# Performance work log

Hardware: AMD Instinct MI355X
Metric: run time of the kernel (lower is better)

Reference implementation:

```python
import jax, jax.numpy as jnp
import numpy as np

CONF_THRES = 0.5   # self.conf_thres
NMS_THRES = 0.5    # self.nms_thres
PRE_NMS = 2048     # candidates kept before pairwise IoU
MAX_DET = 300      # padded detections returned per image
MAX_WH = 4096.0    # class-offset trick so NMS is per-class
IMG_SIZE = 416.0   # self.img_size; boxes_scale (416,416)->(416,416) => scale 1


def xywh2xyxy(b):
    xy, wh = b[..., :2], b[..., 2:4]
    return jnp.concatenate([xy - wh * 0.5, xy + wh * 0.5], axis=-1)


def pairwise_iou(boxes):
    # boxes: [K,4] xyxy -> [K,K] IoU
    area = (boxes[:, 2] - boxes[:, 0]) * (boxes[:, 3] - boxes[:, 1])
    lt = jnp.maximum(boxes[:, None, :2], boxes[None, :, :2])
    rb = jnp.minimum(boxes[:, None, 2:], boxes[None, :, 2:])
    wh = jnp.clip(rb - lt, 0.0)
    inter = wh[..., 0] * wh[..., 1]
    return inter / (area[:, None] + area[None, :] - inter + 1e-16)


def nms_single(pred):
    # pred: [N,85] = xywh(4) + objectness(1) + class scores(80)
    boxes = xywh2xyxy(pred[:, :4])
    obj = pred[:, 4]
    cls_scores = pred[:, 5:] * obj[:, None]        # conf = obj * class prob
    conf = jnp.max(cls_scores, axis=-1)
    cls_id = jnp.argmax(cls_scores, axis=-1)
    valid = obj >= CONF_THRES                      # confidence threshold filter
    score = jnp.where(valid, conf, -1.0)

    order = jnp.argsort(-score)[:PRE_NMS]          # sort desc, keep top PRE_NMS
    boxes_s = boxes[order]
    score_s = score[order]
    cls_s = cls_id[order]
    valid_s = valid[order]

    # per-class NMS via coordinate offset by class id
    off = cls_s.astype(boxes_s.dtype) * MAX_WH
    iou = pairwise_iou(boxes_s + off[:, None])     # [PRE_NMS, PRE_NMS]

    def body(keep, i):
        suppressed = jnp.any(keep & (iou[:, i] > NMS_THRES))
        k = valid_s[i] & ~suppressed
        return keep.at[i].set(k), k

    keep, _ = jax.lax.scan(body, jnp.zeros(PRE_NMS, dtype=bool), jnp.arange(PRE_NMS))

    final_score = jnp.where(keep, score_s, -1.0)
    top = jnp.argsort(-final_score)[:MAX_DET]
    kb, ks, kc, km = boxes_s[top], score_s[top], cls_s[top], keep[top]

    scale = IMG_SIZE / 416.0                       # boxes_scale (identity here)
    det = jnp.concatenate(
        [kb * scale, ks[:, None], kc[:, None].astype(kb.dtype)], axis=-1)
    return jnp.where(km[:, None], det, 0.0)        # [MAX_DET, 6] padded


def setup_inputs() -> dict:
    key = jax.random.key(0)
    predictions = jax.random.uniform(key, (16, 10647, 85), dtype=jnp.float32)
    return {"predictions": predictions}


def reference(predictions):
    # detections per image: [x1,y1,x2,y2,score,class], zero-padded to MAX_DET
    return jax.vmap(nms_single)(predictions)  # [B, MAX_DET, 6]
```

## Files before the change

kernel.cpp:

```cpp
#include <hip/hip_runtime.h>
#include <hip/hip_bf16.h>
#include <stdint.h>

typedef unsigned long long u64;
typedef unsigned int u32;
typedef unsigned short u16;

#define NANCH 10647
#define NBATCH 16
#define NSORT 16384
#define NSEL 2048
#define NWORD 32
#define NCLS 80
#define CONF_T 0.5f
#define NMS_T 0.5f
#define MAXDET 300
#define MAXWH 4096.0f
#define CANDCAP 10688
#define PART 1344
#define NBLK1 84

__device__ __forceinline__ float dec_score(u64 key) {
    u32 v = ~(u32)(key >> 32);
    u32 u = (v & 0x80000000u) ? (v & 0x7FFFFFFFu) : ~v;
    return __uint_as_float(u);
}

__global__ __launch_bounds__(256) void k_prep(const float* __restrict__ pred,
                                              u64* __restrict__ keys,
                                              float4* __restrict__ boxes,
                                              int* __restrict__ cls,
                                              u32* __restrict__ bhist,
                                              u32* __restrict__ ghist2) {
    __shared__ float sm[128 * 85];
    __shared__ u32 ph[256];
    int b = blockIdx.y;
    if (blockIdx.x == 0) ghist2[(size_t)b * 256 + threadIdx.x] = 0;
    int a0 = blockIdx.x * 128;
    int na = NANCH - a0; if (na > 128) na = 128;
    const float* src = pred + ((size_t)b * NANCH + a0) * 85;
    int tot = na * 85;
    ph[threadIdx.x] = 0;
    {
        size_t srcaddr = (size_t)src;
        int shift = (int)((srcaddr & 15) >> 2);
        const float4* A = (const float4*)(srcaddr & ~(size_t)15);
        int nvec = (tot + shift + 3) >> 2;
        for (int j = threadIdx.x; j < nvec; j += 256) {
            float4 v = A[j];
            int base = 4 * j - shift;
            if (base >= 0 && base + 3 < tot) {
                sm[base] = v.x; sm[base + 1] = v.y;
                sm[base + 2] = v.z; sm[base + 3] = v.w;
            } else {
                if (base >= 0 && base < tot)         sm[base]     = v.x;
                if (base + 1 >= 0 && base + 1 < tot) sm[base + 1] = v.y;
                if (base + 2 >= 0 && base + 2 < tot) sm[base + 2] = v.z;
                if (base + 3 >= 0 && base + 3 < tot) sm[base + 3] = v.w;
            }
        }
    }
    __syncthreads();
    int t = threadIdx.x;
    u64 kk = 0;
    if (t < na) {
        const float* s = &sm[t * 85];
        float x = s[0], y = s[1], w = s[2], h = s[3], obj = s[4];
        float best = s[5] * obj; int arg = 0;
        #pragma unroll
        for (int c = 1; c < 80; ++c) {
            float v = s[5 + c] * obj;
            if (v > best) { best = v; arg = c; }
        }
        bool valid = obj >= CONF_T;
        float sc = valid ? best : -1.0f;
        int a = a0 + t;
        float4 bx;
        bx.x = x - w * 0.5f; bx.y = y - h * 0.5f;
        bx.z = x + w * 0.5f; bx.w = y + h * 0.5f;
        size_t o = (size_t)b * NANCH + a;
        boxes[o] = bx;
        cls[o] = arg;
        u32 u = __float_as_uint(sc);
        u32 v = (u & 0x80000000u) ? ~u : (u | 0x80000000u);
        u32 hi = ~v;
        kk = ((u64)hi << 32) | (u32)a;
        keys[(size_t)b * NSORT + a] = kk;
    }
    u32 bin = (t < na) ? (u32)(kk >> 56) : 0xFFFFFFFFu;
    int lane = t & 63;
    u64 rem = __ballot(t < na);
    while (rem) {
        int srcl = __ffsll((long long)rem) - 1;
        u32 lb = __shfl(bin, srcl);
        u64 same = __ballot(bin == lb) & rem;
        if (lane == srcl) atomicAdd(&ph[lb], (u32)__popcll(same));
        rem &= ~same;
    }
    __syncthreads();
    bhist[(((size_t)b * NBLK1) + blockIdx.x) * 256 + threadIdx.x] = ph[threadIdx.x];
}

__global__ __launch_bounds__(1024) void k_scan(const u64* __restrict__ keys,
                                               const u32* __restrict__ bhist,
                                               u64* __restrict__ gslice,
                                               uint2* __restrict__ gpart,
                                               u32* __restrict__ ghist2) {
    __shared__ u32 hist[256];
    __shared__ u32 hsc[256];
    __shared__ u32 ph2[256];
    __shared__ u32 s_D0;
    __shared__ u32 wcs[16], wcc[16];
    __shared__ u32 s_tc;
    int b = blockIdx.y;
    int part = blockIdx.x;
    int tid = threadIdx.x;
    int lane = tid & 63, wv = tid >> 6;
    u64 below = (1ULL << lane) - 1ULL;
    const u64* KB = keys + (size_t)b * NSORT;

    if (tid < 256) {
        ph2[tid] = 0;
        u32 h = 0;
        const u32* BH = bhist + (size_t)b * NBLK1 * 256 + tid;
        for (int j = 0; j < NBLK1; ++j) h += BH[(size_t)j * 256];
        hist[tid] = h;
    }
    __syncthreads();
    if (tid < 64) {
        u32 h0 = hist[tid*4], h1 = hist[tid*4+1], h2 = hist[tid*4+2], h3 = hist[tid*4+3];
        u32 loc = h0 + h1 + h2 + h3;
        u32 p = loc;
        #pragma unroll
        for (int o = 1; o < 64; o <<= 1) { u32 t2 = __shfl_up(p, o); if (lane >= o) p += t2; }
        u32 base = p - loc;
        hsc[tid*4]   = base + h0;
        hsc[tid*4+1] = base + h0 + h1;
        hsc[tid*4+2] = base + h0 + h1 + h2;
        hsc[tid*4+3] = base + h0 + h1 + h2 + h3;
    }
    __syncthreads();
    if (tid < 256) {
        u32 inc = hsc[tid], cb = inc - hist[tid];
        if (cb < NSEL && NSEL <= inc) s_D0 = tid;
    }
    __syncthreads();
    u32 D0 = s_D0;

    u64 kk0 = 0, kk1 = 0;
    bool s0 = false, s1 = false, c0 = false, c1 = false;
    {
        int off = tid, i = part * PART + off;
        bool inb = (off < PART) && (i < NANCH);
        kk0 = inb ? KB[i] : 0ULL;
        u32 top = (u32)(kk0 >> 56);
        s0 = inb && (top < D0); c0 = inb && (top == D0);
    }
    {
        int off = 1024 + tid, i = part * PART + off;
        bool inb = (off < PART) && (i < NANCH);
        kk1 = inb ? KB[i] : 0ULL;
        u32 top = (u32)(kk1 >> 56);
        s1 = inb && (top < D0); c1 = inb && (top == D0);
    }
    if (c0) atomicAdd(&ph2[(u32)(kk0 >> 48) & 0xFFu], 1u);
    if (c1) atomicAdd(&ph2[(u32)(kk1 >> 48) & 0xFFu], 1u);
    u64 bs0 = __ballot(s0), bs1 = __ballot(s1);
    u64 bc0 = __ballot(c0), bc1 = __ballot(c1);
    if (lane == 0) {
        wcs[wv] = (u32)(__popcll(bs0) + __popcll(bs1));
        wcc[wv] = (u32)(__popcll(bc0) + __popcll(bc1));
    }
    __syncthreads();
    if (tid < 16) {
        u32 vs = wcs[tid], vc = wcc[tid];
        u32 ps = vs, pc = vc;
        #pragma unroll
        for (int o = 1; o < 16; o <<= 1) {
            u32 ts = __shfl_up(ps, o);
            u32 tc = __shfl_up(pc, o);
            if (tid >= o) { ps += ts; pc += tc; }
        }
        wcs[tid] = ps - vs;
        wcc[tid] = pc - vc;
        if (tid == 15) {
            s_tc = pc;
            gpart[(size_t)b * 8 + part] = make_uint2(ps, pc);
        }
    }
    __syncthreads();
    u64* SL = gslice + ((size_t)b * 8 + part) * (size_t)PART;
    u32 base_s = wcs[wv];
    u32 base_c = (u32)PART - s_tc + wcc[wv];
    if (s0) SL[base_s + __popcll(bs0 & below)] = kk0;
    if (s1) SL[base_s + __popcll(bs0) + __popcll(bs1 & below)] = kk1;
    if (c0) SL[base_c + __popcll(bc0 & below)] = kk0;
    if (c1) SL[base_c + __popcll(bc0) + __popcll(bc1 & below)] = kk1;
    if (tid < 256 && ph2[tid]) atomicAdd(&ghist2[(size_t)b * 256 + tid], ph2[tid]);
}

__global__ __launch_bounds__(1024) void k_fin(const u64* __restrict__ gslice,
                                              const uint2* __restrict__ gpart,
                                              const u32* __restrict__ ghist2,
                                              u64* __restrict__ gskey,
                                              u64* __restrict__ gkeep) {
    __shared__ u64 sk[NSEL];
    __shared__ u64 cand[CANDCAP];
    __shared__ u32 hist[256];
    __shared__ u32 hsc[256];
    __shared__ u64 s_red[16];
    __shared__ u32 ssA[8], ccA[8];
    __shared__ u32 s_D, s_r0, s_rank, s_cnt, s_cand;

    int b = blockIdx.x;
    int tid = threadIdx.x;
    int lane = tid & 63, wv = tid >> 6;
    u64 below = (1ULL << lane) - 1ULL;

    if (tid < 8) { uint2 v = gpart[(size_t)b * 8 + tid]; ssA[tid] = v.x; ccA[tid] = v.y; }
    if (tid < 256) hist[tid] = ghist2[(size_t)b * 256 + tid];
    for (int i = tid; i < NSEL; i += 1024) sk[i] = ~0ULL;
    __syncthreads();
    if (tid == 0) {
        u32 a = 0;
        for (int j = 0; j < 8; ++j) a += ssA[j];
        s_r0 = NSEL - a;
        s_cnt = 0; s_cand = 0;
    }
    if (tid < 64) {
        u32 h0 = hist[tid*4], h1 = hist[tid*4+1], h2 = hist[tid*4+2], h3 = hist[tid*4+3];
        u32 loc = h0 + h1 + h2 + h3;
        u32 p = loc;
        #pragma unroll
        for (int o = 1; o < 64; o <<= 1) { u32 t2 = __shfl_up(p, o); if (lane >= o) p += t2; }
        u32 base = p - loc;
        hsc[tid*4]   = base + h0;
        hsc[tid*4+1] = base + h0 + h1;
        hsc[tid*4+2] = base + h0 + h1 + h2;
        hsc[tid*4+3] = base + h0 + h1 + h2 + h3;
    }
    __syncthreads();
    if (tid < 256) {
        u32 inc = hsc[tid], cb = inc - hist[tid];
        u32 r0 = s_r0;
        if (cb < r0 && r0 <= inc) s_D = tid;
    }
    __syncthreads();
    u32 D48 = s_D;

    if (wv < 8) {
        int j = wv;
        const u64* SL = gslice + ((size_t)b * 8 + j) * (size_t)PART;
        u32 ns = ssA[j];
        for (u32 i0 = 0; i0 < ns; i0 += 64) {
            u32 i = i0 + lane;
            bool act = i < ns;
            u64 kk = act ? SL[i] : 0ULL;
            u64 bal = __ballot(act);
            u32 base = 0;
            if (lane == 0) base = atomicAdd(&s_cnt, (u32)__popcll(bal));
            base = __shfl(base, 0);
            if (act) sk[base + __popcll(bal & below)] = kk;
        }
    } else {
        int j = wv - 8;
        u32 nc = ccA[j];
        const u64* SL = gslice + ((size_t)b * 8 + j) * (size_t)PART + (PART - nc);
        for (u32 i0 = 0; i0 < nc; i0 += 64) {
            u32 i = i0 + lane;
            bool act = i < nc;
            u64 kk = act ? SL[i] : 0ULL;
            u32 dg = (u32)(kk >> 48) & 0xFFu;
            bool tks = act && (dg < D48);
            bool tkc = act && (dg == D48);
            u64 bs = __ballot(tks), bc = __ballot(tkc);
            u32 base_s = 0, base_c = 0;
            if (lane == 0) {
                if (bs) base_s = atomicAdd(&s_cnt, (u32)__popcll(bs));
                if (bc) base_c = atomicAdd(&s_cand, (u32)__popcll(bc));
            }
            base_s = __shfl(base_s, 0); base_c = __shfl(base_c, 0);
            if (tks) sk[base_s + __popcll(bs & below)] = kk;
            if (tkc) cand[base_c + __popcll(bc & below)] = kk;
        }
    }
    __syncthreads();
    if (tid == 0) s_rank = NSEL - s_cnt;
    __syncthreads();

    const int shifts2[5] = {48, 40, 32, 8, 0};
    for (int rr = 1; ; ++rr) {
        u32 cn = s_cand, r = s_rank;
        if (r == cn || rr == 5) {
            for (u32 i0 = 0; i0 < cn; i0 += 1024) {
                u32 i = i0 + tid;
                bool take = i < cn;
                u64 kk = take ? cand[i] : 0ULL;
                u64 bt = __ballot(take);
                u32 base = 0;
                if (lane == 0 && bt) base = atomicAdd(&s_cnt, (u32)__popcll(bt));
                base = __shfl(base, 0);
                if (take) sk[base + __popcll(bt & below)] = kk;
            }
            break;
        }
        if (r == 1) {
            u64 best = ~0ULL;
            for (u32 i = tid; i < cn; i += 1024) { u64 kk = cand[i]; if (kk < best) best = kk; }
            #pragma unroll
            for (int o = 32; o > 0; o >>= 1) {
                u64 other = __shfl_down(best, o);
                if (other < best) best = other;
            }
            if (lane == 0) s_red[tid >> 6] = best;
            __syncthreads();
            if (tid == 0) {
                u64 m = s_red[0];
                for (int w2 = 1; w2 < 16; ++w2) if (s_red[w2] < m) m = s_red[w2];
                sk[atomicAdd(&s_cnt, 1u)] = m;
            }
            break;
        }
        int shift = shifts2[rr];
        if (tid < 256) hist[tid] = 0;
        __syncthreads();
        for (u32 i = tid; i < cn; i += 1024)
            atomicAdd(&hist[(u32)(cand[i] >> shift) & 0xFFu], 1u);
        __syncthreads();
        if (tid < 64) {
            u32 h0 = hist[tid*4], h1 = hist[tid*4+1], h2 = hist[tid*4+2], h3 = hist[tid*4+3];
            u32 loc = h0 + h1 + h2 + h3;
            u32 p = loc;
            #pragma unroll
            for (int o = 1; o < 64; o <<= 1) { u32 t2 = __shfl_up(p, o); if (lane >= o) p += t2; }
            u32 base = p - loc;
            hsc[tid*4]   = base + h0;
            hsc[tid*4+1] = base + h0 + h1;
            hsc[tid*4+2] = base + h0 + h1 + h2;
            hsc[tid*4+3] = base + h0 + h1 + h2 + h3;
        }
        __syncthreads();
        if (tid < 256) {
            u32 inc = hsc[tid], cb = inc - hist[tid];
            if (cb < r && r <= inc) { s_D = tid; s_rank = r - cb; }
        }
        __syncthreads();
        u32 D = s_D;
        u64 vv[11]; bool vb[11];
        #pragma unroll
        for (int it = 0; it < 11; ++it) {
            u32 i = tid + it * 1024;
            vb[it] = (i < cn);
            vv[it] = vb[it] ? cand[i] : 0ULL;
        }
        __syncthreads();
        if (tid == 0) s_cand = 0;
        __syncthreads();
        #pragma unroll
        for (int it = 0; it < 11; ++it) {
            u32 dg = (u32)(vv[it] >> shift) & 0xFFu;
            bool tk = vb[it] && (dg < D);
            u64 bt = __ballot(tk);
            u32 base = 0;
            if (lane == 0 && bt) base = atomicAdd(&s_cnt, (u32)__popcll(bt));
            base = __shfl(base, 0);
            if (tk) sk[base + __popcll(bt & below)] = vv[it];
        }
        #pragma unroll
        for (int it = 0; it < 11; ++it) {
            u32 dg = (u32)(vv[it] >> shift) & 0xFFu;
            bool tk = vb[it] && (dg == D);
            u64 bt = __ballot(tk);
            u32 base = 0;
            if (lane == 0 && bt) base = atomicAdd(&s_cand, (u32)__popcll(bt));
            base = __shfl(base, 0);
            if (tk) cand[base + __popcll(bt & below)] = vv[it];
        }
        __syncthreads();
    }
    __syncthreads();

    {
        int w = tid >> 6, l = lane;
        int base = w * 128;
        u64 a = sk[base + l], c = sk[base + 64 + l];
        #pragma unroll
        for (int k = 2; k <= 128; k <<= 1) {
            for (int j = k >> 1; j > 0; j >>= 1) {
                if (j == 64) {
                    bool dir = (((base + l) & k) == 0);
                    u64 lo = a < c ? a : c;
                    u64 hi = a < c ? c : a;
                    a = dir ? lo : hi;
                    c = dir ? hi : lo;
                } else {
                    bool up_ = (l & j) != 0;
                    bool dira = (((base + l) & k) == 0);
                    bool dirc = (((base + 64 + l) & k) == 0);
                    u64 pa = __shfl_xor(a, j);
                    u64 pc = __shfl_xor(c, j);
                    a = (up_ == dira) ? (a > pa ? a : pa) : (a < pa ? a : pa);
                    c = (up_ == dirc) ? (c > pc ? c : pc) : (c < pc ? c : pc);
                }
            }
        }
        sk[base + l] = a; sk[base + 64 + l] = c;
        __syncthreads();
        for (int k = 256; k <= NSEL; k <<= 1) {
            for (int j = k >> 1; j >= 128; j >>= 1) {
                int n = tid;
                int i = ((n & ~(j - 1)) << 1) | (n & (j - 1));
                int l2 = i | j;
                u64 x = sk[i], y = sk[l2];
                bool up2 = ((i & k) == 0);
                if ((x > y) == up2) { sk[i] = y; sk[l2] = x; }
                __syncthreads();
            }
            a = sk[base + l]; c = sk[base + 64 + l];
            bool dirk = ((base & k) == 0);
            {
                u64 lo = a < c ? a : c;
                u64 hi = a < c ? c : a;
                a = dirk ? lo : hi;
                c = dirk ? hi : lo;
            }
            #pragma unroll
            for (int j = 32; j > 0; j >>= 1) {
                bool up_ = (l & j) != 0;
                u64 pa = __shfl_xor(a, j);
                u64 pc = __shfl_xor(c, j);
                a = (up_ == dirk) ? (a > pa ? a : pa) : (a < pa ? a : pa);
                c = (up_ == dirk) ? (c > pc ? c : pc) : (c < pc ? c : pc);
            }
            sk[base + l] = a; sk[base + 64 + l] = c;
            __syncthreads();
        }
    }

    for (int i = tid; i < NSEL; i += 1024) gskey[(size_t)b * NSEL + i] = sk[i];
    if (tid < NWORD) gkeep[(size_t)b * NWORD + tid] = 0ULL;
}

__global__ __launch_bounds__(256) void k_gather(const u64* __restrict__ gskey,
                                                const float4* __restrict__ boxes,
                                                const int* __restrict__ cls,
                                                float4* __restrict__ sel_box,
                                                float4* __restrict__ sel_sbox,
                                                float* __restrict__ sel_area,
                                                float* __restrict__ sel_score,
                                                int* __restrict__ sel_cls) {
    int b = blockIdx.y;
    int r = blockIdx.x * 256 + threadIdx.x;
    u64 key = gskey[(size_t)b * NSEL + r];
    int a = (int)(key & 0xFFFFFFFFu);
    if ((unsigned)a >= NANCH) a = 0;
    size_t src = (size_t)b * NANCH + a;
    float4 bx = boxes[src];
    int c = cls[src];
    float sc = dec_score(key);
    float off = (float)c * MAXWH;
    float4 sb;
    sb.x = bx.x + off; sb.y = bx.y + off;
    sb.z = bx.z + off; sb.w = bx.w + off;
    float area = (sb.z - sb.x) * (sb.w - sb.y);
    size_t o = (size_t)b * NSEL + r;
    sel_box[o] = bx; sel_sbox[o] = sb; sel_area[o] = area;
    sel_score[o] = sc; sel_cls[o] = c;
}

__global__ __launch_bounds__(1024) void k_cnms(const float4* __restrict__ sel_sbox,
                                               const float* __restrict__ sel_area,
                                               const int* __restrict__ sel_cls,
                                               const float* __restrict__ sel_score,
                                               u64* __restrict__ gkeep) {
    __shared__ u16 wmem[16][NSEL];
    __shared__ u64 wkeep[16][NWORD];

    int b = blockIdx.y;
    int cg = blockIdx.x;
    int lane = threadIdx.x & 63, wv = threadIdx.x >> 6;
    int c = cg * 16 + wv;
    size_t bb = (size_t)b * NSEL;
    const int* CL = sel_cls + bb;
    const float* SC = sel_score + bb;
    u64 below = (1ULL << lane) - 1ULL;

    int n = 0;
    for (int ch = 0; ch < NWORD; ++ch) {
        int i = ch * 64 + lane;
        bool pred = (CL[i] == c) && (SC[i] >= 0.0f);
        u64 bal = __ballot(pred);
        if (pred) wmem[wv][n + __popcll(bal & below)] = (u16)i;
        n += __popcll(bal);
    }

    for (int c0 = 0; c0 < n; c0 += 64) {
        int chunkn = n - c0; if (chunkn > 64) chunkn = 64;
        bool mv = lane < chunkn;
        int q = mv ? (int)wmem[wv][c0 + lane] : 0;
        float4 bq = sel_sbox[bb + q];
        float aq = sel_area[bb + q];

        bool hit = false;
        for (int j = 0; j < c0; ++j) {
            if (!((wkeep[wv][j >> 6] >> (j & 63)) & 1ULL)) continue;
            int p = (int)wmem[wv][j];
            float4 bp = sel_sbox[bb + p];
            float ap = sel_area[bb + p];
            float ltx = fmaxf(bp.x, bq.x), lty = fmaxf(bp.y, bq.y);
            float rbx = fminf(bp.z, bq.z), rby = fminf(bp.w, bq.w);
            float ww = fmaxf(rbx - ltx, 0.0f), hh = fmaxf(rby - lty, 0.0f);
            float inter = ww * hh;
            hit = hit || (mv && (inter / (ap + aq - inter + 1e-16f) > NMS_T));
        }
        u64 avail = __ballot(mv && !hit);

        u64 Rt = 0;
        for (int t = 0; t < chunkn; ++t) {
            int p = (int)wmem[wv][c0 + t];
            float4 bp = sel_sbox[bb + p];
            float ap = sel_area[bb + p];
            float ltx = fmaxf(bp.x, bq.x), lty = fmaxf(bp.y, bq.y);
            float rbx = fminf(bp.z, bq.z), rby = fminf(bp.w, bq.w);
            float ww = fmaxf(rbx - ltx, 0.0f), hh = fmaxf(rby - lty, 0.0f);
            float inter = ww * hh;
            u64 row = __ballot(mv && (inter / (ap + aq - inter + 1e-16f) > NMS_T));
            if (lane == t) Rt = row;
        }

        u64 U = avail, kept = 0;
        while (U) {
            bool inU = ((U >> lane) & 1ULL) != 0ULL;
            u64 newk = __ballot(inU && ((Rt & U & below) == 0ULL));
            u64 killed = __ballot((Rt & newk) != 0ULL);
            kept |= newk;
            U &= ~(newk | killed);
        }
        if (lane == 0) wkeep[wv][c0 >> 6] = kept;
        if ((kept >> lane) & 1ULL)
            atomicOr(&gkeep[(size_t)b * NWORD + (q >> 6)], 1ULL << (q & 63));
    }
}

__global__ __launch_bounds__(64) void k_out(const u64* __restrict__ gkeep,
                                            const float4* __restrict__ sel_box,
                                            const float* __restrict__ sel_score,
                                            const int* __restrict__ sel_cls,
                                            float* __restrict__ out) {
    int b = blockIdx.x;
    int lane = threadIdx.x;
    const float* SC = sel_score + (size_t)b * NSEL;
    u64 kreg = (lane < NWORD) ? gkeep[(size_t)b * NWORD + lane] : 0ULL;

    int cnt = (lane < NWORD) ? __popcll(kreg) : 0;
    int pre = cnt;
    #pragma unroll
    for (int dd = 1; dd < 64; dd <<= 1) {
        int o = __shfl_up(pre, dd);
        if (lane >= dd) pre += o;
    }
    int total = __shfl(pre, 63);
    int base = pre - cnt;
    float* OUT = out + (size_t)b * MAXDET * 6;
    if (lane < NWORD) {
        u64 m = kreg;
        int rr = 0;
        while (m) {
            int t = __ffsll((long long)m) - 1;
            m &= m - 1;
            int slot = base + rr; ++rr;
            if (slot < MAXDET) {
                int i = lane * 64 + t;
                size_t src = (size_t)b * NSEL + i;
                float4 bx = sel_box[src];
                float sc = SC[i];
                int c = sel_cls[src];
                float* o6 = OUT + slot * 6;
                o6[0] = bx.x; o6[1] = bx.y; o6[2] = bx.z; o6[3] = bx.w;
                o6[4] = sc; o6[5] = (float)c;
            }
        }
    }
    int start = total > MAXDET ? MAXDET : total;
    for (int s = start + lane; s < MAXDET; s += 64) {
        float* o6 = OUT + s * 6;
        o6[0] = 0.0f; o6[1] = 0.0f; o6[2] = 0.0f;
        o6[3] = 0.0f; o6[4] = 0.0f; o6[5] = 0.0f;
    }
}

extern "C" void kernel_launch(void* const* d_in, const int* in_sizes, int n_in,
                              void* d_out, int out_size, void* d_ws, size_t ws_size,
                              hipStream_t stream) {
    const float* pred = (const float*)d_in[0];
    float* out = (float*)d_out;

    char* ws = (char*)d_ws;
    size_t off = 0;
    auto alloc = [&](size_t bytes) -> void* {
        void* p = ws + off;
        off += (bytes + 255) & ~(size_t)255;
        return p;
    };

    u64*    keys      = (u64*)   alloc((size_t)NBATCH * NSORT * 8);
    float4* boxes     = (float4*)alloc((size_t)NBATCH * NANCH * 16);
    int*    cls       = (int*)   alloc((size_t)NBATCH * NANCH * 4);
    u32*    bhist     = (u32*)   alloc((size_t)NBATCH * NBLK1 * 256 * 4);
    u32*    ghist2    = (u32*)   alloc((size_t)NBATCH * 256 * 4);
    u64*    gslice    = (u64*)   alloc((size_t)NBATCH * 8 * PART * 8);
    uint2*  gpart     = (uint2*) alloc((size_t)NBATCH * 8 * 8);
    u64*    gskey     = (u64*)   alloc((size_t)NBATCH * NSEL * 8);
    u64*    gkeep     = (u64*)   alloc((size_t)NBATCH * NWORD * 8);
    float4* sel_box   = (float4*)alloc((size_t)NBATCH * NSEL * 16);
    float4* sel_sbox  = (float4*)alloc((size_t)NBATCH * NSEL * 16);
    float*  sel_area  = (float*) alloc((size_t)NBATCH * NSEL * 4);
    float*  sel_score = (float*) alloc((size_t)NBATCH * NSEL * 4);
    int*    sel_cls   = (int*)   alloc((size_t)NBATCH * NSEL * 4);

    dim3 g1(NBLK1, NBATCH);
    k_prep<<<g1, 256, 0, stream>>>(pred, keys, boxes, cls, bhist, ghist2);

    dim3 g2(8, NBATCH);
    k_scan<<<g2, 1024, 0, stream>>>(keys, bhist, gslice, gpart, ghist2);

    k_fin<<<NBATCH, 1024, 0, stream>>>(gslice, gpart, ghist2, gskey, gkeep);

    dim3 g4(8, NBATCH);
    k_gather<<<g4, 256, 0, stream>>>(gskey, boxes, cls,
                                     sel_box, sel_sbox, sel_area,
                                     sel_score, sel_cls);

    dim3 g5(5, NBATCH);
    k_cnms<<<g5, 1024, 0, stream>>>(sel_sbox, sel_area, sel_cls, sel_score, gkeep);

    k_out<<<NBATCH, 64, 0, stream>>>(gkeep, sel_box, sel_score, sel_cls, out);
}
```

Baseline: 100.5 us.

## Fuse gather into class-NMS kernel with compacted shared-memory box staging

Removes the separate gather kernel and its intermediate selection buffers. The NMS kernel now reads sorted keys, boxes and classes directly, does a two-pass count and prefix sum to compact each class's candidates into one shared pool, and stages the offset boxes and areas in LDS. The inner IoU loops then read from shared memory instead of global memory. The output kernel decodes score, box and class from the key again. The cost is one fewer launch and less global traffic, in exchange for reading the keys twice and doing dependent global loads on the class array.

New measurement: 134.2 us. 1.33x slower.

```diff
diff --git a/kernel.cpp b/kernel.cpp
--- a/kernel.cpp
+++ b/kernel.cpp
@@ -441,72 +441,81 @@
     if (tid < NWORD) gkeep[(size_t)b * NWORD + tid] = 0ULL;
 }
 
-__global__ __launch_bounds__(256) void k_gather(const u64* __restrict__ gskey,
-                                                const float4* __restrict__ boxes,
-                                                const int* __restrict__ cls,
-                                                float4* __restrict__ sel_box,
-                                                float4* __restrict__ sel_sbox,
-                                                float* __restrict__ sel_area,
-                                                float* __restrict__ sel_score,
-                                                int* __restrict__ sel_cls) {
-    int b = blockIdx.y;
-    int r = blockIdx.x * 256 + threadIdx.x;
-    u64 key = gskey[(size_t)b * NSEL + r];
-    int a = (int)(key & 0xFFFFFFFFu);
-    if ((unsigned)a >= NANCH) a = 0;
-    size_t src = (size_t)b * NANCH + a;
-    float4 bx = boxes[src];
-    int c = cls[src];
-    float sc = dec_score(key);
-    float off = (float)c * MAXWH;
-    float4 sb;
-    sb.x = bx.x + off; sb.y = bx.y + off;
-    sb.z = bx.z + off; sb.w = bx.w + off;
-    float area = (sb.z - sb.x) * (sb.w - sb.y);
-    size_t o = (size_t)b * NSEL + r;
-    sel_box[o] = bx; sel_sbox[o] = sb; sel_area[o] = area;
-    sel_score[o] = sc; sel_cls[o] = c;
-}
-
-__global__ __launch_bounds__(1024) void k_cnms(const float4* __restrict__ sel_sbox,
-                                               const float* __restrict__ sel_area,
-                                               const int* __restrict__ sel_cls,
-                                               const float* __restrict__ sel_score,
+__global__ __launch_bounds__(1024) void k_cnms(const u64* __restrict__ gskey,
+                                               const float4* __restrict__ boxes,
+                                               const int* __restrict__ cls,
                                                u64* __restrict__ gkeep) {
-    __shared__ u16 wmem[16][NSEL];
+    __shared__ u16 pool[NSEL];
+    __shared__ float4 sbox[NSEL];
+    __shared__ float sar[NSEL];
+    __shared__ u32 cnt16[16], base16[16];
     __shared__ u64 wkeep[16][NWORD];
 
     int b = blockIdx.y;
     int cg = blockIdx.x;
     int lane = threadIdx.x & 63, wv = threadIdx.x >> 6;
     int c = cg * 16 + wv;
-    size_t bb = (size_t)b * NSEL;
-    const int* CL = sel_cls + bb;
-    const float* SC = sel_score + bb;
+    const u64* KY = gskey + (size_t)b * NSEL;
+    const float4* BX = boxes + (size_t)b * NANCH;
+    const int* CL = cls + (size_t)b * NANCH;
     u64 below = (1ULL << lane) - 1ULL;
+    float off = (float)c * MAXWH;
 
     int n = 0;
     for (int ch = 0; ch < NWORD; ++ch) {
         int i = ch * 64 + lane;
-        bool pred = (CL[i] == c) && (SC[i] >= 0.0f);
+        u64 key = KY[i];
+        bool valid = (key >> 63) == 0ULL;
+        int a = (int)(key & 0xFFFFFFFFu);
+        int ci = valid ? CL[a] : -1;
+        n += __popcll(__ballot(ci == c));
+    }
+    if (lane == 0) cnt16[wv] = (u32)n;
+    __syncthreads();
+    if (wv == 0 && lane < 16) {
+        u32 v = cnt16[lane];
+        u32 p = v;
+        #pragma unroll
+        for (int o = 1; o < 16; o <<= 1) { u32 t2 = __shfl_up(p, o); if (lane >= o) p += t2; }
+        base16[lane] = p - v;
+    }
+    __syncthreads();
+
+    u32 run = base16[wv];
+    for (int ch = 0; ch < NWORD; ++ch) {
+        int i = ch * 64 + lane;
+        u64 key = KY[i];
+        bool valid = (key >> 63) == 0ULL;
+        int a = (int)(key & 0xFFFFFFFFu);
+        int ci = valid ? CL[a] : -1;
+        bool pred = (ci == c);
         u64 bal = __ballot(pred);
-        if (pred) wmem[wv][n + __popcll(bal & below)] = (u16)i;
-        n += __popcll(bal);
-    }
+        if (pred) {
+            u32 pos = run + __popcll(bal & below);
+            pool[pos] = (u16)i;
+            float4 b4 = BX[a];
+            float4 sb;
+            sb.x = b4.x + off; sb.y = b4.y + off;
+            sb.z = b4.z + off; sb.w = b4.w + off;
+            sbox[pos] = sb;
+            sar[pos] = (sb.z - sb.x) * (sb.w - sb.y);
+        }
+        run += (u32)__popcll(bal);
+    }
+    u32 nb = base16[wv];
 
     for (int c0 = 0; c0 < n; c0 += 64) {
         int chunkn = n - c0; if (chunkn > 64) chunkn = 64;
         bool mv = lane < chunkn;
-        int q = mv ? (int)wmem[wv][c0 + lane] : 0;
-        float4 bq = sel_sbox[bb + q];
-        float aq = sel_area[bb + q];
+        u32 qp = nb + c0 + (mv ? lane : 0);
+        float4 bq = sbox[qp];
+        float aq = sar[qp];
 
         bool hit = false;
         for (int j = 0; j < c0; ++j) {
             if (!((wkeep[wv][j >> 6] >> (j & 63)) & 1ULL)) continue;
-            int p = (int)wmem[wv][j];
-            float4 bp = sel_sbox[bb + p];
-            float ap = sel_area[bb + p];
+            float4 bp = sbox[nb + j];
+            float ap = sar[nb + j];
             float ltx = fmaxf(bp.x, bq.x), lty = fmaxf(bp.y, bq.y);
             float rbx = fminf(bp.z, bq.z), rby = fminf(bp.w, bq.w);
             float ww = fmaxf(rbx - ltx, 0.0f), hh = fmaxf(rby - lty, 0.0f);
@@ -517,9 +526,8 @@
 
         u64 Rt = 0;
         for (int t = 0; t < chunkn; ++t) {
-            int p = (int)wmem[wv][c0 + t];
-            float4 bp = sel_sbox[bb + p];
-            float ap = sel_area[bb + p];
+            float4 bp = sbox[nb + c0 + t];
+            float ap = sar[nb + c0 + t];
             float ltx = fmaxf(bp.x, bq.x), lty = fmaxf(bp.y, bq.y);
             float rbx = fminf(bp.z, bq.z), rby = fminf(bp.w, bq.w);
             float ww = fmaxf(rbx - ltx, 0.0f), hh = fmaxf(rby - lty, 0.0f);
@@ -537,19 +545,21 @@
             U &= ~(newk | killed);
         }
         if (lane == 0) wkeep[wv][c0 >> 6] = kept;
-        if ((kept >> lane) & 1ULL)
+        if ((kept >> lane) & 1ULL) {
+            int q = (int)pool[nb + c0 + lane];
             atomicOr(&gkeep[(size_t)b * NWORD + (q >> 6)], 1ULL << (q & 63));
+        }
     }
 }
 
 __global__ __launch_bounds__(64) void k_out(const u64* __restrict__ gkeep,
-                                            const float4* __restrict__ sel_box,
-                                            const float* __restrict__ sel_score,
-                                            const int* __restrict__ sel_cls,
+                                            const u64* __restrict__ gskey,
+                                            const float4* __restrict__ boxes,
+                                            const int* __restrict__ cls,
                                             float* __restrict__ out) {
     int b = blockIdx.x;
     int lane = threadIdx.x;
-    const float* SC = sel_score + (size_t)b * NSEL;
+    const u64* KY = gskey + (size_t)b * NSEL;
     u64 kreg = (lane < NWORD) ? gkeep[(size_t)b * NWORD + lane] : 0ULL;
 
     int cnt = (lane < NWORD) ? __popcll(kreg) : 0;
@@ -571,10 +581,12 @@
             int slot = base + rr; ++rr;
             if (slot < MAXDET) {
                 int i = lane * 64 + t;
-                size_t src = (size_t)b * NSEL + i;
-                float4 bx = sel_box[src];
-                float sc = SC[i];
-                int c = sel_cls[src];
+                u64 key = KY[i];
+                int a = (int)(key & 0xFFFFFFFFu);
+                if ((unsigned)a >= NANCH) a = 0;
+                float4 bx = boxes[(size_t)b * NANCH + a];
+                int c = cls[(size_t)b * NANCH + a];
+                float sc = dec_score(key);
                 float* o6 = OUT + slot * 6;
                 o6[0] = bx.x; o6[1] = bx.y; o6[2] = bx.z; o6[3] = bx.w;
                 o6[4] = sc; o6[5] = (float)c;
@@ -603,20 +615,15 @@
         return p;
     };
 
-    u64*    keys      = (u64*)   alloc((size_t)NBATCH * NSORT * 8);
-    float4* boxes     = (float4*)alloc((size_t)NBATCH * NANCH * 16);
-    int*    cls       = (int*)   alloc((size_t)NBATCH * NANCH * 4);
-    u32*    bhist     = (u32*)   alloc((size_t)NBATCH * NBLK1 * 256 * 4);
-    u32*    ghist2    = (u32*)   alloc((size_t)NBATCH * 256 * 4);
-    u64*    gslice    = (u64*)   alloc((size_t)NBATCH * 8 * PART * 8);
-    uint2*  gpart     = (uint2*) alloc((size_t)NBATCH * 8 * 8);
-    u64*    gskey     = (u64*)   alloc((size_t)NBATCH * NSEL * 8);
-    u64*    gkeep     = (u64*)   alloc((size_t)NBATCH * NWORD * 8);
-    float4* sel_box   = (float4*)alloc((size_t)NBATCH * NSEL * 16);
-    float4* sel_sbox  = (float4*)alloc((size_t)NBATCH * NSEL * 16);
-    float*  sel_area  = (float*) alloc((size_t)NBATCH * NSEL * 4);
-    float*  sel_score = (float*) alloc((size_t)NBATCH * NSEL * 4);
-    int*    sel_cls   = (int*)   alloc((size_t)NBATCH * NSEL * 4);
+    u64*    keys   = (u64*)   alloc((size_t)NBATCH * NSORT * 8);
+    float4* boxes  = (float4*)alloc((size_t)NBATCH * NANCH * 16);
+    int*    cls    = (int*)   alloc((size_t)NBATCH * NANCH * 4);
+    u32*    bhist  = (u32*)   alloc((size_t)NBATCH * NBLK1 * 256 * 4);
+    u32*    ghist2 = (u32*)   alloc((size_t)NBATCH * 256 * 4);
+    u64*    gslice = (u64*)   alloc((size_t)NBATCH * 8 * PART * 8);
+    uint2*  gpart  = (uint2*) alloc((size_t)NBATCH * 8 * 8);
+    u64*    gskey  = (u64*)   alloc((size_t)NBATCH * NSEL * 8);
+    u64*    gkeep  = (u64*)   alloc((size_t)NBATCH * NWORD * 8);
 
     dim3 g1(NBLK1, NBATCH);
     k_prep<<<g1, 256, 0, stream>>>(pred, keys, boxes, cls, bhist, ghist2);
@@ -626,13 +633,8 @@
 
     k_fin<<<NBATCH, 1024, 0, stream>>>(gslice, gpart, ghist2, gskey, gkeep);
 
-    dim3 g4(8, NBATCH);
-    k_gather<<<g4, 256, 0, stream>>>(gskey, boxes, cls,
-                                     sel_box, sel_sbox, sel_area,
-                                     sel_score, sel_cls);
-
-    dim3 g5(5, NBATCH);
-    k_cnms<<<g5, 1024, 0, stream>>>(sel_sbox, sel_area, sel_cls, sel_score, gkeep);
-
-    k_out<<<NBATCH, 64, 0, stream>>>(gkeep, sel_box, sel_score, sel_cls, out);
+    dim3 g4(5, NBATCH);
+    k_cnms<<<g4, 1024, 0, stream>>>(gskey, boxes, cls, gkeep);
+
+    k_out<<<NBATCH, 64, 0, stream>>>(gkeep, gskey, boxes, cls, out);
 }
```
